# Performance work log

Hardware: AMD Instinct MI355X
Metric: run time of the kernel (lower is better)

The kernel has to match this reference:

```python
import jax, jax.numpy as jnp
import numpy as np

HIDDEN = 2560
N_HEADS = 16
N_KV = 4
HEAD_DIM = 256
GQA = N_HEADS // N_KV
INNER = N_HEADS * HEAD_DIM  # 4096
B, L = 2, 2048
ROPE_THETA = 1000000.0
EPS = 1e-6


def _rope_tables(seq_len, dim, theta):
    pos = np.arange(seq_len, dtype=np.float32)
    inv_freq = 1.0 / (theta ** (np.arange(0, dim, 2, dtype=np.float32) / dim))
    ang = pos[:, None] * inv_freq[None, :]          # [L, dim/2]
    ang = np.concatenate([ang, ang], axis=-1)        # [L, dim]
    return jnp.asarray(np.cos(ang)), jnp.asarray(np.sin(ang))


def setup_inputs() -> dict:
    key = jax.random.key(0)
    ks = jax.random.split(key, 6)
    hidden_states = jax.random.normal(ks[0], (B, L, HIDDEN), dtype=jnp.float32)
    cos, sin = _rope_tables(L, HEAD_DIM, ROPE_THETA)
    s = 0.02
    Wq = jax.random.normal(ks[1], (HIDDEN, 2 * INNER), dtype=jnp.float32) * s
    Wk = jax.random.normal(ks[2], (HIDDEN, N_KV * HEAD_DIM), dtype=jnp.float32) * s
    Wv = jax.random.normal(ks[3], (HIDDEN, N_KV * HEAD_DIM), dtype=jnp.float32) * s
    Wo = jax.random.normal(ks[4], (INNER, HIDDEN), dtype=jnp.float32) * s
    q_norm_w = jnp.ones((HEAD_DIM,), dtype=jnp.float32)
    k_norm_w = jnp.ones((HEAD_DIM,), dtype=jnp.float32)
    return {"hidden_states": hidden_states, "cos": cos, "sin": sin,
            "Wq": Wq, "Wk": Wk, "Wv": Wv, "Wo": Wo,
            "q_norm_w": q_norm_w, "k_norm_w": k_norm_w}


def _rms_norm(x, w):
    var = jnp.mean(jnp.square(x), axis=-1, keepdims=True)
    return x * jax.lax.rsqrt(var + EPS) * w


def _apply_rotary(x, cos, sin):
    # x: [B, H, L, D]; cos/sin: [L, D]
    d = x.shape[-1]
    x1, x2 = x[..., : d // 2], x[..., d // 2:]
    return x * cos + jnp.concatenate([-x2, x1], axis=-1) * sin


def reference(hidden_states, cos, sin, Wq, Wk, Wv, Wo, q_norm_w, k_norm_w):
    Bv, Lv, _ = hidden_states.shape
    qg = hidden_states @ Wq                              # [B, L, 2*INNER]
    q, gate = qg[..., :INNER], qg[..., INNER:]
    k = (hidden_states @ Wk).reshape(Bv, Lv, N_KV, HEAD_DIM)
    v = (hidden_states @ Wv).reshape(Bv, Lv, N_KV, HEAD_DIM)

    q = _rms_norm(q.reshape(Bv, Lv, N_HEADS, HEAD_DIM), q_norm_w).transpose(0, 2, 1, 3)  # [B,H,L,D]
    k = _rms_norm(k, k_norm_w).transpose(0, 2, 1, 3)     # [B,KV,L,D]
    v = v.transpose(0, 2, 1, 3)                          # [B,KV,L,D]

    q = _apply_rotary(q, cos, sin)
    k = _apply_rotary(k, cos, sin)

    # repeat_interleave over head dim for GQA
    k = jnp.repeat(k, GQA, axis=1)                       # [B,H,L,D]
    v = jnp.repeat(v, GQA, axis=1)

    scale = 1.0 / jnp.sqrt(jnp.float32(HEAD_DIM))
    scores = jnp.einsum('bhqd,bhkd->bhqk', q, k) * scale  # [B,H,L,L]
    causal = jnp.tril(jnp.ones((Lv, Lv), dtype=bool))
    scores = jnp.where(causal, scores, jnp.finfo(scores.dtype).min)
    attn = jax.nn.softmax(scores, axis=-1)
    out = jnp.einsum('bhqk,bhkd->bhqd', attn, v)          # [B,H,L,D]

    out = out.transpose(0, 2, 1, 3).reshape(Bv, Lv, INNER) * jax.nn.silu(gate)
    return out @ Wo
```

## Files before the change

### kernel.cpp

```cpp
#include <hip/hip_runtime.h>
#include <cstdint>
#include <cstddef>

#define NQKV 10240

typedef __bf16 bf16;
typedef __attribute__((ext_vector_type(4))) __bf16 bvec4;
typedef __attribute__((ext_vector_type(8))) __bf16 bvec8;
typedef __attribute__((ext_vector_type(4))) float fvec4;

__device__ __forceinline__ void gll16(const bf16* g, bf16* l) {
  __builtin_amdgcn_global_load_lds(
      (const __attribute__((address_space(1))) void*)g,
      (__attribute__((address_space(3))) void*)l, 16, 0, 0);
}

__global__ __launch_bounds__(256) void cvt_f32_bf16(const float* __restrict__ x,
                                                    bf16* __restrict__ y, int n) {
  int i = (blockIdx.x * 256 + threadIdx.x) * 4;
  if (i < n) {
    float4 v = *(const float4*)(x + i);
    bvec4 o;
    o.x = (bf16)v.x; o.y = (bf16)v.y; o.z = (bf16)v.z; o.w = (bf16)v.w;
    *(bvec4*)(y + i) = o;
  }
}

__global__ __launch_bounds__(256) void wtrans(const float* __restrict__ W,
                                              bf16* __restrict__ Wt, int K, int N) {
  __shared__ float t[64][65];
  int n0 = blockIdx.x * 64, k0 = blockIdx.y * 64;
  int tx = threadIdx.x & 63, tg = threadIdx.x >> 6;
#pragma unroll
  for (int i = 0; i < 16; ++i) {
    int r = tg * 16 + i;
    t[r][tx] = W[(size_t)(k0 + r) * N + n0 + tx];
  }
  __syncthreads();
#pragma unroll
  for (int i = 0; i < 16; ++i) {
    int r = tg * 16 + i;
    Wt[(size_t)(n0 + r) * K + k0 + tx] = (bf16)t[tx][r];
  }
}

__global__ __launch_bounds__(256) void vtrans(const bf16* __restrict__ QKV,
                                              bf16* __restrict__ Vt) {
  __shared__ bf16 t[64][65];
  int l0 = blockIdx.x * 64, dd0 = blockIdx.y * 64;
  int bkv = blockIdx.z, b = bkv >> 2, kv = bkv & 3;
  int tx = threadIdx.x & 63, tg = threadIdx.x >> 6;
#pragma unroll
  for (int i = 0; i < 16; ++i) {
    int r = tg * 16 + i;
    t[r][tx] = QKV[(size_t)(b * 2048 + l0 + r) * NQKV + 9216 + kv * 256 + dd0 + tx];
  }
  __syncthreads();
#pragma unroll
  for (int i = 0; i < 16; ++i) {
    int r = tg * 16 + i;
    Vt[((size_t)bkv * 256 + dd0 + r) * 2048 + l0 + tx] = t[tx][r];
  }
}

__global__ __launch_bounds__(256) void norm_rope(const bf16* __restrict__ QKV,
    const float* __restrict__ cosT, const float* __restrict__ sinT,
    const float* __restrict__ qw, const float* __restrict__ kw,
    bf16* __restrict__ Qn, bf16* __restrict__ Kn) {
  int u = blockIdx.x * 4 + (threadIdx.x >> 6);
  int lane = threadIdx.x & 63;
  int token = u / 20, slot = u - token * 20;
  int b = token >> 11, l = token & 2047;
  int d0 = lane * 4;
  const float* w;
  int col0;
  bf16* outp;
  if (slot < 16) {
    col0 = slot * 256; w = qw;
    outp = Qn + ((size_t)((b * 16 + slot) * 2048 + l)) * 256;
  } else {
    int kv = slot - 16;
    col0 = 8192 + kv * 256; w = kw;
    outp = Kn + ((size_t)((b * 4 + kv) * 2048 + l)) * 256;
  }
  bvec4 xi = *(const bvec4*)(QKV + (size_t)token * NQKV + col0 + d0);
  float x[4];
#pragma unroll
  for (int j = 0; j < 4; ++j) x[j] = (float)xi[j];
  float ss = x[0] * x[0] + x[1] * x[1] + x[2] * x[2] + x[3] * x[3];
#pragma unroll
  for (int off = 32; off; off >>= 1) ss += __shfl_xor(ss, off);
  float rn = rsqrtf(ss * (1.0f / 256.0f) + 1e-6f);
  float xn[4];
#pragma unroll
  for (int j = 0; j < 4; ++j) xn[j] = x[j] * rn * w[d0 + j];
  bvec4 o;
#pragma unroll
  for (int j = 0; j < 4; ++j) {
    float other = __shfl_xor(xn[j], 32);
    float rot = (lane < 32) ? -other : other;
    float c = cosT[(size_t)l * 256 + d0 + j];
    float s = sinT[(size_t)l * 256 + d0 + j];
    o[j] = (bf16)(xn[j] * c + rot * s);
  }
  *(bvec4*)(outp + d0) = o;
}

template <typename OutT>
__global__ __launch_bounds__(256) void gemm_bt(const bf16* __restrict__ A,
                                               const bf16* __restrict__ B,
                                               OutT* __restrict__ C,
                                               int N, int Kd) {
  __shared__ alignas(16) bf16 As[4096];
  __shared__ alignas(16) bf16 Bs[4096];
  int tid = threadIdx.x, wave = tid >> 6, lane = tid & 63;
  int quad = lane >> 4, l15 = lane & 15;
  int wm = wave >> 1, wn = wave & 1;
  int m0 = blockIdx.y * 128, n0 = blockIdx.x * 128;
  const fvec4 FZ = {0.f, 0.f, 0.f, 0.f};
  fvec4 acc[4][4];
#pragma unroll
  for (int i = 0; i < 4; ++i)
#pragma unroll
    for (int j = 0; j < 4; ++j) acc[i][j] = FZ;
  int ar = lane >> 2;
  int ac = (lane & 3) * 8;
  for (int kt = 0; kt < Kd; kt += 32) {
    __syncthreads();
#pragma unroll
    for (int i = 0; i < 2; ++i) {
      int seg = wave * 2 + i;
      int row = seg * 16 + ar;
      gll16(A + (size_t)(m0 + row) * Kd + kt + ac, As + seg * 512);
      gll16(B + (size_t)(n0 + row) * Kd + kt + ac, Bs + seg * 512);
    }
    __syncthreads();
    bvec8 af[4], bfv[4];
#pragma unroll
    for (int t = 0; t < 4; ++t) {
      af[t]  = *(const bvec8*)(As + (wm * 64 + t * 16 + l15) * 32 + quad * 8);
      bfv[t] = *(const bvec8*)(Bs + (wn * 64 + t * 16 + l15) * 32 + quad * 8);
    }
#pragma unroll
    for (int mt = 0; mt < 4; ++mt)
#pragma unroll
      for (int nt = 0; nt < 4; ++nt)
        acc[mt][nt] = __builtin_amdgcn_mfma_f32_16x16x32_bf16(af[mt], bfv[nt],
                                                              acc[mt][nt], 0, 0, 0);
  }
#pragma unroll
  for (int mt = 0; mt < 4; ++mt)
#pragma unroll
    for (int nt = 0; nt < 4; ++nt)
#pragma unroll
      for (int r = 0; r < 4; ++r) {
        int row = m0 + wm * 64 + mt * 16 + quad * 4 + r;
        int col = n0 + wn * 64 + nt * 16 + l15;
        C[(size_t)row * N + col] = (OutT)acc[mt][nt][r];
      }
}

__global__ __launch_bounds__(256, 2) void flash(const bf16* __restrict__ Q,
    const bf16* __restrict__ K, const bf16* __restrict__ Vt,
    const bf16* __restrict__ QKV, bf16* __restrict__ Og) {
  __shared__ alignas(16) bf16 smem[32768];
  bf16* Ks = smem;
  bf16* Vts = smem + 16384;

  int pairi = blockIdx.x;
  int bh = blockIdx.y, b = bh >> 4, h = bh & 15, kvh = h >> 2;
  int tid = threadIdx.x, wave = tid >> 6, lane = tid & 63;
  int quad = lane >> 4, l15 = lane & 15;

  const bf16* Qh = Q + ((size_t)(b * 16 + h) * 2048) * 256;
  const bf16* Kb = K + ((size_t)(b * 4 + kvh) * 2048) * 256;
  const bf16* Vb = Vt + ((size_t)(b * 4 + kvh) * 256) * 2048;
  const fvec4 FZ = {0.f, 0.f, 0.f, 0.f};

  for (int half = 0; half < 2; ++half) {
    int qt = half ? (31 - pairi) : pairi;
    int q0 = qt * 64;

    bvec8 qf[8];
    {
      int row = q0 + wave * 16 + l15;
#pragma unroll
      for (int kk = 0; kk < 8; ++kk) {
        bvec8 v = *(const bvec8*)(Qh + (size_t)row * 256 + kk * 32 + quad * 8);
#pragma unroll
        for (int j = 0; j < 8; ++j) v[j] = (bf16)((float)v[j] * 0.0625f);
        qf[kk] = v;
      }
    }

    fvec4 acc[16];
#pragma unroll
    for (int i = 0; i < 16; ++i) acc[i] = FZ;
    float m_run[4], l_run[4];
#pragma unroll
    for (int r = 0; r < 4; ++r) { m_run[r] = -3.0e38f; l_run[r] = 0.f; }

    for (int kt = 0; kt <= qt; ++kt) {
      int k0 = kt * 64;
      __syncthreads();
#pragma unroll
      for (int i = 0; i < 8; ++i) {
        int seg = wave * 8 + i;
        int krow = seg * 2 + (lane >> 5);
        int kc = (lane & 31) ^ (krow & 31);
        gll16(Kb + (size_t)(k0 + krow) * 256 + kc * 8, Ks + seg * 512);
        int vrow = seg * 8 + (lane >> 3);
        int vc = (lane & 7) ^ (vrow & 7);
        gll16(Vb + (size_t)vrow * 2048 + k0 + vc * 8, Vts + seg * 512);
      }
      __syncthreads();

      fvec4 s[4];
#pragma unroll
      for (int nt = 0; nt < 4; ++nt) {
        s[nt] = FZ;
        int row = nt * 16 + l15;
        int rm = row & 31;
#pragma unroll
        for (int ks = 0; ks < 8; ++ks) {
          int c = ks * 4 + quad;
          bvec8 kf = *(const bvec8*)(Ks + (size_t)row * 256 + (size_t)(c ^ rm) * 8);
          s[nt] = __builtin_amdgcn_mfma_f32_16x16x32_bf16(qf[ks], kf, s[nt], 0, 0, 0);
        }
      }
      __syncthreads();

      if (kt == qt) {
#pragma unroll
        for (int nt = 0; nt < 4; ++nt)
#pragma unroll
          for (int r = 0; r < 4; ++r)
            if (k0 + nt * 16 + l15 > q0 + wave * 16 + quad * 4 + r)
              s[nt][r] = -3.0e38f;
      }

      bf16* Pw = smem + wave * 1152;
      float alpha[4];
      {
        float rs[4];
#pragma unroll
        for (int r = 0; r < 4; ++r) {
          float m = fmaxf(fmaxf(s[0][r], s[1][r]),
                          fmaxf(s[2][r], s[3][r]));
#pragma unroll
          for (int off = 8; off; off >>= 1) m = fmaxf(m, __shfl_xor(m, off));
          float Mn = fmaxf(m_run[r], m);
          alpha[r] = __expf(m_run[r] - Mn);
          m_run[r] = Mn;
          rs[r] = 0.f;
        }
#pragma unroll
        for (int nt = 0; nt < 4; ++nt)
#pragma unroll
          for (int r = 0; r < 4; ++r) {
            float p = __expf(s[nt][r] - m_run[r]);
            rs[r] += p;
            Pw[(quad * 4 + r) * 72 + nt * 16 + l15] = (bf16)p;
          }
#pragma unroll
        for (int r = 0; r < 4; ++r) {
#pragma unroll
          for (int off = 8; off; off >>= 1) rs[r] += __shfl_xor(rs[r], off);
          l_run[r] = l_run[r] * alpha[r] + rs[r];
        }
#pragma unroll
        for (int nt = 0; nt < 16; ++nt)
#pragma unroll
          for (int r = 0; r < 4; ++r) acc[nt][r] *= alpha[r];
      }
      __syncthreads();

#pragma unroll
      for (int ks = 0; ks < 2; ++ks) {
        bvec8 pf = *(const bvec8*)(Pw + l15 * 72 + ks * 32 + quad * 8);
#pragma unroll
        for (int nt = 0; nt < 16; ++nt) {
          int row = nt * 16 + l15;
          int c = ks * 4 + quad;
          bvec8 vf = *(const bvec8*)(Vts + (size_t)row * 64 + (size_t)(c ^ (row & 7)) * 8);
          acc[nt] = __builtin_amdgcn_mfma_f32_16x16x32_bf16(pf, vf, acc[nt], 0, 0, 0);
        }
      }
    }

#pragma unroll
    for (int r = 0; r < 4; ++r) {
      int token = b * 2048 + q0 + wave * 16 + quad * 4 + r;
      float inv = 1.0f / l_run[r];
#pragma unroll
      for (int nt = 0; nt < 16; ++nt) {
        int col = h * 256 + nt * 16 + l15;
        float g = (float)QKV[(size_t)token * NQKV + 4096 + col];
        float silu = g / (1.0f + __expf(-g));
        Og[(size_t)token * 4096 + col] = (bf16)(acc[nt][r] * inv * silu);
      }
    }
  }
}

extern "C" void kernel_launch(void* const* d_in, const int* in_sizes, int n_in,
                              void* d_out, int out_size, void* d_ws, size_t ws_size,
                              hipStream_t stream) {
  const float* hs   = (const float*)d_in[0];
  const float* cosT = (const float*)d_in[1];
  const float* sinT = (const float*)d_in[2];
  const float* Wq   = (const float*)d_in[3];
  const float* Wk   = (const float*)d_in[4];
  const float* Wv   = (const float*)d_in[5];
  const float* Wo   = (const float*)d_in[6];
  const float* qw   = (const float*)d_in[7];
  const float* kw   = (const float*)d_in[8];
  float* out = (float*)d_out;

  char* p = (char*)d_ws;
  auto alloc = [&](size_t bytes) {
    char* r = p;
    p += (bytes + 255) & ~(size_t)255;
    return r;
  };
  bf16* Xb    = (bf16*)alloc((size_t)4096 * 2560 * 2);
  bf16* Wqkvt = (bf16*)alloc((size_t)10240 * 2560 * 2);
  bf16* Wot   = (bf16*)alloc((size_t)2560 * 4096 * 2);
  bf16* QKV   = (bf16*)alloc((size_t)4096 * 10240 * 2);
  bf16* Qn    = (bf16*)alloc((size_t)2 * 16 * 2048 * 256 * 2);
  bf16* Kn    = (bf16*)alloc((size_t)2 * 4 * 2048 * 256 * 2);
  bf16* Vtb   = (bf16*)alloc((size_t)2 * 4 * 256 * 2048 * 2);
  bf16* Og    = (bf16*)alloc((size_t)4096 * 4096 * 2);

  cvt_f32_bf16<<<10240, 256, 0, stream>>>(hs, Xb, 4096 * 2560);
  wtrans<<<dim3(128, 40), 256, 0, stream>>>(Wq, Wqkvt, 2560, 8192);
  wtrans<<<dim3(16, 40), 256, 0, stream>>>(Wk, Wqkvt + (size_t)8192 * 2560, 2560, 1024);
  wtrans<<<dim3(16, 40), 256, 0, stream>>>(Wv, Wqkvt + (size_t)9216 * 2560, 2560, 1024);
  wtrans<<<dim3(40, 64), 256, 0, stream>>>(Wo, Wot, 4096, 2560);

  gemm_bt<bf16><<<dim3(80, 32), 256, 0, stream>>>(Xb, Wqkvt, QKV, 10240, 2560);

  norm_rope<<<20480, 256, 0, stream>>>(QKV, cosT, sinT, qw, kw, Qn, Kn);
  vtrans<<<dim3(32, 4, 8), 256, 0, stream>>>(QKV, Vtb);

  flash<<<dim3(16, 32), 256, 0, stream>>>(Qn, Kn, Vtb, QKV, Og);

  gemm_bt<float><<<dim3(20, 32), 256, 0, stream>>>(Og, Wot, out, 2560, 4096);
}
```

Before: 849.2 us.

## Rewrite GEMM with 128x256 tiles, triple-buffered async LDS loads and swizzle

Replaces the single-buffered 128x128 GEMM with a 128x256 tile kernel. It uses a three-stage ring of LDS buffers filled by global_load_lds, so the loads for tile t+2 overlap the MFMAs on tile t. The LDS layout is XOR-swizzled to reduce bank conflicts, and s_setprio raises MFMA issue priority. Each wave now holds twice as many accumulators and the kernel targets two blocks per CU. This risks register pressure and leaves fewer blocks per GEMM launch.

```diff
diff --git a/kernel.cpp b/kernel.cpp
--- a/kernel.cpp
+++ b/kernel.cpp
@@ -107,56 +107,96 @@
 }
 
 template <typename OutT>
-__global__ __launch_bounds__(256) void gemm_bt(const bf16* __restrict__ A,
-                                               const bf16* __restrict__ B,
-                                               OutT* __restrict__ C,
-                                               int N, int Kd) {
-  __shared__ alignas(16) bf16 As[4096];
-  __shared__ alignas(16) bf16 Bs[4096];
+__global__ __launch_bounds__(256, 2) void gemm8(const bf16* __restrict__ A,
+                                                const bf16* __restrict__ B,
+                                                OutT* __restrict__ C,
+                                                int N, int Kd) {
+  __shared__ alignas(16) bf16 smem[36864];
   int tid = threadIdx.x, wave = tid >> 6, lane = tid & 63;
   int quad = lane >> 4, l15 = lane & 15;
   int wm = wave >> 1, wn = wave & 1;
-  int m0 = blockIdx.y * 128, n0 = blockIdx.x * 128;
+  int bm = blockIdx.y, bn = blockIdx.x;
+  const bf16* Ag = A + (size_t)bm * 128 * Kd;
+  const bf16* Bg = B + (size_t)bn * 256 * Kd;
+
+  bf16* b0 = smem;
+  bf16* b1 = smem + 12288;
+  bf16* b2 = smem + 24576;
+
+  int nt = Kd >> 5;
+  int srow = lane >> 2;
+  int sc8 = ((lane & 3) ^ ((lane >> 3) & 3)) * 8;
+  int csw = (quad ^ ((l15 >> 1) & 3)) * 8;
+
   const fvec4 FZ = {0.f, 0.f, 0.f, 0.f};
-  fvec4 acc[4][4];
+  fvec4 acc[4][8];
 #pragma unroll
   for (int i = 0; i < 4; ++i)
 #pragma unroll
-    for (int j = 0; j < 4; ++j) acc[i][j] = FZ;
-  int ar = lane >> 2;
-  int ac = (lane & 3) * 8;
-  for (int kt = 0; kt < Kd; kt += 32) {
-    __syncthreads();
-#pragma unroll
-    for (int i = 0; i < 2; ++i) {
-      int seg = wave * 2 + i;
-      int row = seg * 16 + ar;
-      gll16(A + (size_t)(m0 + row) * Kd + kt + ac, As + seg * 512);
-      gll16(B + (size_t)(n0 + row) * Kd + kt + ac, Bs + seg * 512);
+    for (int j = 0; j < 8; ++j) acc[i][j] = FZ;
+
+  auto stage = [&](bf16* dst, int ktel) {
+#pragma unroll
+    for (int i = 0; i < 6; ++i) {
+      int s = wave * 6 + i;
+      if (s < 8) {
+        gll16(Ag + (size_t)(s * 16 + srow) * Kd + ktel + sc8, dst + s * 512);
+      } else {
+        gll16(Bg + (size_t)((s - 8) * 16 + srow) * Kd + ktel + sc8,
+              dst + 4096 + (s - 8) * 512);
+      }
     }
-    __syncthreads();
-    bvec8 af[4], bfv[4];
-#pragma unroll
-    for (int t = 0; t < 4; ++t) {
-      af[t]  = *(const bvec8*)(As + (wm * 64 + t * 16 + l15) * 32 + quad * 8);
-      bfv[t] = *(const bvec8*)(Bs + (wn * 64 + t * 16 + l15) * 32 + quad * 8);
-    }
+  };
+
+  stage(b0, 0);
+  stage(b1, 32);
+
+  for (int t = 0; t < nt; ++t) {
+    asm volatile("s_waitcnt vmcnt(6)" ::: "memory");
+    __builtin_amdgcn_s_barrier();
+    const bf16* Ab = b0;
+    const bf16* Bb = b0 + 4096;
+    bvec8 af[4], bv[8];
 #pragma unroll
     for (int mt = 0; mt < 4; ++mt)
-#pragma unroll
-      for (int nt = 0; nt < 4; ++nt)
-        acc[mt][nt] = __builtin_amdgcn_mfma_f32_16x16x32_bf16(af[mt], bfv[nt],
-                                                              acc[mt][nt], 0, 0, 0);
-  }
+      af[mt] = *(const bvec8*)(Ab + (wm * 64 + mt * 16 + l15) * 32 + csw);
+#pragma unroll
+    for (int nt2 = 0; nt2 < 8; ++nt2)
+      bv[nt2] = *(const bvec8*)(Bb + (wn * 128 + nt2 * 16 + l15) * 32 + csw);
+    __builtin_amdgcn_s_setprio(1);
+#pragma unroll
+    for (int mt = 0; mt < 2; ++mt)
+#pragma unroll
+      for (int nt2 = 0; nt2 < 8; ++nt2)
+        acc[mt][nt2] = __builtin_amdgcn_mfma_f32_16x16x32_bf16(af[mt], bv[nt2],
+                                                               acc[mt][nt2], 0, 0, 0);
+    __builtin_amdgcn_s_setprio(0);
+    asm volatile("s_waitcnt lgkmcnt(0)" ::: "memory");
+    __builtin_amdgcn_sched_barrier(0);
+    __builtin_amdgcn_s_barrier();
+    int t2 = t + 2;
+    if (t2 >= nt) t2 = nt - 1;
+    stage(b2, t2 * 32);
+    __builtin_amdgcn_s_setprio(1);
+#pragma unroll
+    for (int mt = 2; mt < 4; ++mt)
+#pragma unroll
+      for (int nt2 = 0; nt2 < 8; ++nt2)
+        acc[mt][nt2] = __builtin_amdgcn_mfma_f32_16x16x32_bf16(af[mt], bv[nt2],
+                                                               acc[mt][nt2], 0, 0, 0);
+    __builtin_amdgcn_s_setprio(0);
+    bf16* tp = b0; b0 = b1; b1 = b2; b2 = tp;
+  }
+
 #pragma unroll
   for (int mt = 0; mt < 4; ++mt)
 #pragma unroll
-    for (int nt = 0; nt < 4; ++nt)
+    for (int nt2 = 0; nt2 < 8; ++nt2)
 #pragma unroll
       for (int r = 0; r < 4; ++r) {
-        int row = m0 + wm * 64 + mt * 16 + quad * 4 + r;
-        int col = n0 + wn * 64 + nt * 16 + l15;
-        C[(size_t)row * N + col] = (OutT)acc[mt][nt][r];
+        int row = bm * 128 + wm * 64 + mt * 16 + quad * 4 + r;
+        int col = bn * 256 + wn * 128 + nt2 * 16 + l15;
+        C[(size_t)row * N + col] = (OutT)acc[mt][nt2][r];
       }
 }
 
@@ -338,12 +378,12 @@
   wtrans<<<dim3(16, 40), 256, 0, stream>>>(Wv, Wqkvt + (size_t)9216 * 2560, 2560, 1024);
   wtrans<<<dim3(40, 64), 256, 0, stream>>>(Wo, Wot, 4096, 2560);
 
-  gemm_bt<bf16><<<dim3(80, 32), 256, 0, stream>>>(Xb, Wqkvt, QKV, 10240, 2560);
+  gemm8<bf16><<<dim3(40, 32), 256, 0, stream>>>(Xb, Wqkvt, QKV, 10240, 2560);
 
   norm_rope<<<20480, 256, 0, stream>>>(QKV, cosT, sinT, qw, kw, Qn, Kn);
   vtrans<<<dim3(32, 4, 8), 256, 0, stream>>>(QKV, Vtb);
 
   flash<<<dim3(16, 32), 256, 0, stream>>>(Qn, Kn, Vtb, QKV, Og);
 
-  gemm_bt<float><<<dim3(20, 32), 256, 0, stream>>>(Og, Wot, out, 2560, 4096);
-}
+  gemm8<float><<<dim3(10, 32), 256, 0, stream>>>(Og, Wot, out, 2560, 4096);
+}
```

Measured after the change: 764.4 us. -10.0%, faster.
